# Kernel optimization log

Measured on AMD Instinct MI355X. Metric: run time of the kernel, lower is better.

Reference implementation:

```python
import jax, jax.numpy as jnp
import numpy as np

Q_LATTICE = 4      # nested lattice alphabet size
QMAX_ACT = 127.0   # 2**(8-1) - 1 for 8-bit LSQ


def _lattice_quantize(x_blocks, G, Ginv, q):
    # x_blocks: [N, 8] rows are block vectors. Lattice point = z @ G, z integer.
    z = jnp.round(x_blocks @ Ginv)
    half = q // 2
    z_mod = jnp.mod(z + half, q) - half  # nested (mod-q) lattice, centered
    return z_mod @ G


def setup_inputs() -> dict:
    key = jax.random.key(0)
    k1, k2 = jax.random.split(key)
    O, I, BS = 4096, 4096, 8
    rng = np.random.default_rng(0)
    G_np = np.eye(BS, dtype=np.float64) + 0.1 * rng.standard_normal((BS, BS))
    Ginv_np = np.linalg.inv(G_np)
    return {
        "x": jax.random.normal(k1, (256, I), dtype=jnp.float32),
        "weight": jax.random.normal(k2, (O, I), dtype=jnp.float32),
        "bias": jnp.zeros((O,), dtype=jnp.float32),
        "theta_beta": jnp.ones((O, 1), dtype=jnp.float32),
        "alpha": jnp.ones((1,), dtype=jnp.float32),
        "G": jnp.asarray(G_np, dtype=jnp.float32),
        "Ginv": jnp.asarray(Ginv_np, dtype=jnp.float32),
    }


def reference(x, weight, bias, theta_beta, alpha, G, Ginv):
    O, I = weight.shape
    bs = G.shape[0]
    nblk = I // bs
    sg = jax.lax.stop_gradient

    # --- hierarchical nested-lattice weight quantization (row tiling) ---
    W_blocks = weight.reshape(O, nblk, bs)
    # theta_beta [O, k] -> mean over k -> [O, 1, 1], broadcast to all blocks
    scale_w = jnp.mean(theta_beta, axis=-1, keepdims=True)[:, None, :]
    W_scaled = (W_blocks * scale_w).reshape(-1, bs)
    # straight-through lattice quantize
    W_q = W_scaled + sg(_lattice_quantize(W_scaled, G, Ginv, Q_LATTICE) - W_scaled)
    W_q = W_q.reshape(O, I)

    # --- linear ---
    y = x @ W_q.T + bias

    # --- LSQ activation quantization ---
    a = jax.nn.relu(alpha) + 1e-8          # [1]
    y_clipped = y + sg(jnp.clip(y, -a, a) - y)  # ste_clip (clamp detached)
    s = a / QMAX_ACT
    y_scaled = y_clipped / s
    y_round = y_scaled + sg(jnp.round(y_scaled) - y_scaled)  # ste_round
    return y_round * s
```

## Files before the change

kernel.cpp:

```cpp
#include <hip/hip_runtime.h>

typedef __attribute__((ext_vector_type(8))) __bf16 bf16x8;
typedef __attribute__((ext_vector_type(4))) float f32x4;

#define M_ 256
#define N_ 4096
#define K_ 4096
#define SPLITK 4
#define KC (K_ / SPLITK)
#define BM 128
#define BN 64
#define BK 32
#define KSTEPS (KC / BK)



__device__ __forceinline__ unsigned short f2bf(float f) {
  unsigned int u = __builtin_bit_cast(unsigned int, f);
  u += 0x7fffu + ((u >> 16) & 1u);
  return (unsigned short)(u >> 16);
}

__device__ __forceinline__ float lsq1(float y, float a, float s) {
  float yc = fminf(fmaxf(y, -a), a);
  return rintf(yc / s) * s;
}

__device__ __forceinline__ bf16x8 zdec_pk(unsigned int w) {
  unsigned int d0, d1, d2, d3;
#define ZP(P, D)                                                        \
  {                                                                     \
    const float f0 = (float)((w >> (4 * P)) & 3u) - 2.0f;               \
    const float f1 = (float)((w >> (4 * P + 2)) & 3u) - 2.0f;           \
    asm("v_cvt_pk_bf16_f32 %0, %1, %2" : "=v"(D) : "v"(f0), "v"(f1));   \
  }
  ZP(0, d0) ZP(1, d1) ZP(2, d2) ZP(3, d3)
#undef ZP
  const uint4 u = make_uint4(d0, d1, d2, d3);
  return __builtin_bit_cast(bf16x8, u);
}


#define NQB ((N_ * K_ / 8) / 256)
#define NXB ((M_ * K_ / 8) / 256)

__global__ __launch_bounds__(256) void k_prep(const float* __restrict__ W,
                                              const float* __restrict__ theta,
                                              const float* __restrict__ Ginv,
                                              const float* __restrict__ x,
                                              const float* __restrict__ G,
                                              unsigned short* __restrict__ z2,
                                              unsigned short* __restrict__ hi,
                                              unsigned short* __restrict__ lo,
                                              int kTheta) {
  __shared__ float Ms[64];
  const int tid = threadIdx.x;
  const bool isQ = blockIdx.x < NQB;
  if (tid < 64) Ms[tid] = isQ ? Ginv[tid] : G[tid];
  __syncthreads();

  if (isQ) {
#pragma clang fp contract(off)
    const int s = blockIdx.x * 256 + tid;
    const int lane6 = s & 63;
    const int tile = s >> 6;
    const int o  = ((tile >> 7) << 4) + (lane6 & 15);
    const int kb = ((tile & 127) << 2) + (lane6 >> 4);
    const float4* wp = (const float4*)(W + ((size_t)o << 12) + ((size_t)kb << 3));
    const float4 w0 = wp[0], w1 = wp[1];
    float sc = 0.f;
    for (int t = 0; t < kTheta; ++t) sc += theta[o * kTheta + t];
    sc /= (float)kTheta;
    const float wsv[8] = {w0.x * sc, w0.y * sc, w0.z * sc, w0.w * sc,
                          w1.x * sc, w1.y * sc, w1.z * sc, w1.w * sc};
    unsigned int word = 0u;
#pragma unroll
    for (int i = 0; i < 8; ++i) {
      float t = 0.f;
#pragma unroll
      for (int j = 0; j < 8; ++j)
        t = t + wsv[j] * Ms[j * 8 + i];
      const int zi = (int)rintf(t);
      word |= (unsigned int)((zi + 2) & 3) << (2 * i);
    }
    z2[s] = (unsigned short)word;
  } else {
    const int s = (blockIdx.x - NQB) * 256 + tid;
    const int lane6 = s & 63;
    const int tile = s >> 6;
    const int m  = ((tile >> 7) << 4) + (lane6 & 15);
    const int kb = ((tile & 127) << 2) + (lane6 >> 4);
    const float4* xp = (const float4*)(x + ((size_t)m << 12) + ((size_t)kb << 3));
    const float4 a0 = xp[0], a1 = xp[1];
    float xv[8] = {a0.x, a0.y, a0.z, a0.w, a1.x, a1.y, a1.z, a1.w};
    unsigned int ph[4] = {0u, 0u, 0u, 0u}, pl[4] = {0u, 0u, 0u, 0u};
#pragma unroll
    for (int i = 0; i < 8; ++i) {
      float t = 0.f;
#pragma unroll
      for (int j = 0; j < 8; ++j) t = fmaf(xv[j], Ms[i * 8 + j], t);
      const unsigned short hb = f2bf(t);
      const float hf = __builtin_bit_cast(float, (unsigned int)hb << 16);
      const unsigned short lb = f2bf(t - hf);
      ph[i >> 1] |= ((unsigned int)hb) << ((i & 1) * 16);
      pl[i >> 1] |= ((unsigned int)lb) << ((i & 1) * 16);
    }
    *(uint4*)(hi + ((size_t)s << 3)) = make_uint4(ph[0], ph[1], ph[2], ph[3]);
    *(uint4*)(lo + ((size_t)s << 3)) = make_uint4(pl[0], pl[1], pl[2], pl[3]);
  }
}


__global__ __launch_bounds__(512, 2) void k_gemm(const unsigned short* __restrict__ xgh,
                                                 const unsigned short* __restrict__ xgl,
                                                 const unsigned short* __restrict__ z2,
                                                 float* __restrict__ part) {
  const int tid = threadIdx.x;
  const int lane = tid & 63, wave = tid >> 6;
  const int wr = wave >> 1, wc = wave & 1;
  const int b = blockIdx.x;
  const int mt = b & 1;
  const int sk = (b >> 1) & 3;
  const int nt = b >> 3;
  const int k0t = sk * (KC / 32);
  const int lrow = lane & 15, lkg = lane >> 4;

  const unsigned short* ab[2];
  const unsigned short* lb2[2];
#pragma unroll
  for (int mf = 0; mf < 2; ++mf) {
    const size_t t = (size_t)((mt * 8 + wr * 2 + mf) * 128 + k0t);
    ab[mf]  = xgh + (t << 9) + lane * 8;
    lb2[mf] = xgl + (t << 9) + lane * 8;
  }
  const unsigned short* zb[2];
#pragma unroll
  for (int nf = 0; nf < 2; ++nf)
    zb[nf] = z2 + (((size_t)((nt * 4 + wc * 2 + nf) * 128 + k0t)) << 6) + lane;

  f32x4 acc[2][2] = {};

  bf16x8 cah[2], cal[2];
  unsigned int czw[2];
#pragma unroll
  for (int mf = 0; mf < 2; ++mf) {
    cah[mf] = *(const bf16x8*)(ab[mf]);
    cal[mf] = *(const bf16x8*)(lb2[mf]);
  }
#pragma unroll
  for (int nf = 0; nf < 2; ++nf) czw[nf] = zb[nf][0];

  for (int ks = 0; ks < KSTEPS; ++ks) {
    bf16x8 nah[2], nal[2];
    unsigned int nzw[2];
    if (ks + 1 < KSTEPS) {
#pragma unroll
      for (int mf = 0; mf < 2; ++mf) {
        nah[mf] = *(const bf16x8*)(ab[mf] + (size_t)(ks + 1) * 512);
        nal[mf] = *(const bf16x8*)(lb2[mf] + (size_t)(ks + 1) * 512);
      }
#pragma unroll
      for (int nf = 0; nf < 2; ++nf) nzw[nf] = zb[nf][(size_t)(ks + 1) * 64];
    } else {
#pragma unroll
      for (int mf = 0; mf < 2; ++mf) { nah[mf] = cah[mf]; nal[mf] = cal[mf]; }
#pragma unroll
      for (int nf = 0; nf < 2; ++nf) nzw[nf] = czw[nf];
    }

    bf16x8 bfr[2];
#pragma unroll
    for (int nf = 0; nf < 2; ++nf) bfr[nf] = zdec_pk(czw[nf]);

#pragma unroll
    for (int mf = 0; mf < 2; ++mf)
#pragma unroll
      for (int nf = 0; nf < 2; ++nf) {
        acc[mf][nf] = __builtin_amdgcn_mfma_f32_16x16x32_bf16(cah[mf], bfr[nf], acc[mf][nf], 0, 0, 0);
        acc[mf][nf] = __builtin_amdgcn_mfma_f32_16x16x32_bf16(cal[mf], bfr[nf], acc[mf][nf], 0, 0, 0);
      }

#pragma unroll
    for (int mf = 0; mf < 2; ++mf) { cah[mf] = nah[mf]; cal[mf] = nal[mf]; }
#pragma unroll
    for (int nf = 0; nf < 2; ++nf) czw[nf] = nzw[nf];
  }

  float* pb = part + (size_t)sk * (M_ * N_);
#pragma unroll
  for (int mf = 0; mf < 2; ++mf)
#pragma unroll
    for (int nf = 0; nf < 2; ++nf)
#pragma unroll
      for (int r = 0; r < 4; ++r) {
        const int m = mt * BM + wr * 32 + mf * 16 + lkg * 4 + r;
        const int n = nt * BN + wc * 32 + nf * 16 + lrow;
        pb[(size_t)m * N_ + n] = acc[mf][nf][r];
      }
}


__global__ __launch_bounds__(256) void k_epi(const float* __restrict__ part,
                                             const float* __restrict__ bias,
                                             const float* __restrict__ alpha,
                                             float* __restrict__ out) {
  const int i4 = blockIdx.x * 256 + threadIdx.x;
  const size_t off = (size_t)i4 * 4;
  const float4 p0 = *(const float4*)(part + off);
  const float4 p1 = *(const float4*)(part + (size_t)1 * M_ * N_ + off);
  const float4 p2 = *(const float4*)(part + (size_t)2 * M_ * N_ + off);
  const float4 p3 = *(const float4*)(part + (size_t)3 * M_ * N_ + off);
  const int n = (int)(off & (N_ - 1));
  const float4 bv = *(const float4*)(bias + n);
  const float a = fmaxf(alpha[0], 0.f) + 1e-8f;
  const float s = a / 127.0f;
  float4 o;
  o.x = lsq1(((p0.x + p1.x) + p2.x) + p3.x + bv.x, a, s);
  o.y = lsq1(((p0.y + p1.y) + p2.y) + p3.y + bv.y, a, s);
  o.z = lsq1(((p0.z + p1.z) + p2.z) + p3.z + bv.z, a, s);
  o.w = lsq1(((p0.w + p1.w) + p2.w) + p3.w + bv.w, a, s);
  *(float4*)(out + off) = o;
}


extern "C" void kernel_launch(void* const* d_in, const int* in_sizes, int n_in,
                              void* d_out, int out_size, void* d_ws, size_t ws_size,
                              hipStream_t stream) {
  const float* x     = (const float*)d_in[0];
  const float* W     = (const float*)d_in[1];
  const float* bias  = (const float*)d_in[2];
  const float* theta = (const float*)d_in[3];
  const float* alpha = (const float*)d_in[4];
  const float* G     = (const float*)d_in[5];
  const float* Ginv  = (const float*)d_in[6];
  float* out = (float*)d_out;

  const int O = in_sizes[2];
  const int kTheta = in_sizes[3] / O;

  char* ws = (char*)d_ws;
  unsigned short* xgh = (unsigned short*)ws;
  unsigned short* xgl = (unsigned short*)(ws + 2097152);
  unsigned short* z2  = (unsigned short*)(ws + 4194304);
  float* part = (float*)(ws + 8388608);
  if (ws_size < 25165824) return;

  k_prep<<<NQB + NXB, 256, 0, stream>>>(W, theta, Ginv, x, G, z2, xgh, xgl, kTheta);
  k_gemm<<<2 * SPLITK * 64, 512, 0, stream>>>(xgh, xgl, z2, part);
  k_epi<<<(M_ * N_ / 4) / 256, 256, 0, stream>>>(part, bias, alpha, out);
}
```

Baseline: 51.24 us.

## Drop split-K and fuse bias/LSQ epilogue into GEMM kernel

```diff
diff --git a/kernel.cpp b/kernel.cpp
--- a/kernel.cpp
+++ b/kernel.cpp
@@ -6,12 +6,10 @@
 #define M_ 256
 #define N_ 4096
 #define K_ 4096
-#define SPLITK 4
-#define KC (K_ / SPLITK)
-#define BM 128
+#define BM 64
 #define BN 64
-#define BK 32
-#define KSTEPS (KC / BK)
+#define NSTEP 128
+#define QSTEP 32
 
 
 
@@ -114,112 +112,73 @@
 __global__ __launch_bounds__(512, 2) void k_gemm(const unsigned short* __restrict__ xgh,
                                                  const unsigned short* __restrict__ xgl,
                                                  const unsigned short* __restrict__ z2,
-                                                 float* __restrict__ part) {
+                                                 const float* __restrict__ bias,
+                                                 const float* __restrict__ alpha,
+                                                 float* __restrict__ out) {
   const int tid = threadIdx.x;
   const int lane = tid & 63, wave = tid >> 6;
   const int wr = wave >> 1, wc = wave & 1;
   const int b = blockIdx.x;
-  const int mt = b & 1;
-  const int sk = (b >> 1) & 3;
-  const int nt = b >> 3;
-  const int k0t = sk * (KC / 32);
+  const int mt = b & 3;
+  const int nt = b >> 2;
   const int lrow = lane & 15, lkg = lane >> 4;
 
-  const unsigned short* ab[2];
-  const unsigned short* lb2[2];
-#pragma unroll
-  for (int mf = 0; mf < 2; ++mf) {
-    const size_t t = (size_t)((mt * 8 + wr * 2 + mf) * 128 + k0t);
-    ab[mf]  = xgh + (t << 9) + lane * 8;
-    lb2[mf] = xgl + (t << 9) + lane * 8;
-  }
+  const size_t ta = (size_t)((mt * 4 + wr) * 128) << 9;
+  const unsigned short* ah_p = xgh + ta + lane * 8;
+  const unsigned short* al_p = xgl + ta + lane * 8;
   const unsigned short* zb[2];
 #pragma unroll
   for (int nf = 0; nf < 2; ++nf)
-    zb[nf] = z2 + (((size_t)((nt * 4 + wc * 2 + nf) * 128 + k0t)) << 6) + lane;
-
-  f32x4 acc[2][2] = {};
-
-  bf16x8 cah[2], cal[2];
-  unsigned int czw[2];
-#pragma unroll
-  for (int mf = 0; mf < 2; ++mf) {
-    cah[mf] = *(const bf16x8*)(ab[mf]);
-    cal[mf] = *(const bf16x8*)(lb2[mf]);
-  }
-#pragma unroll
-  for (int nf = 0; nf < 2; ++nf) czw[nf] = zb[nf][0];
-
-  for (int ks = 0; ks < KSTEPS; ++ks) {
-    bf16x8 nah[2], nal[2];
-    unsigned int nzw[2];
-    if (ks + 1 < KSTEPS) {
-#pragma unroll
-      for (int mf = 0; mf < 2; ++mf) {
-        nah[mf] = *(const bf16x8*)(ab[mf] + (size_t)(ks + 1) * 512);
-        nal[mf] = *(const bf16x8*)(lb2[mf] + (size_t)(ks + 1) * 512);
+    zb[nf] = z2 + (((size_t)((nt * 4 + wc * 2 + nf) * 128)) << 6) + lane;
+
+  f32x4 acc[4][2] = {};
+
+  bf16x8 cah = *(const bf16x8*)(ah_p);
+  bf16x8 cal = *(const bf16x8*)(al_p);
+  unsigned int czw[2] = {zb[0][0], zb[1][0]};
+
+#pragma unroll
+  for (int q = 0; q < 4; ++q) {
+    for (int t = 0; t < QSTEP; ++t) {
+      const int ks = q * QSTEP + t;
+      bf16x8 nah, nal;
+      unsigned int nzw[2];
+      if (ks + 1 < NSTEP) {
+        nah = *(const bf16x8*)(ah_p + (size_t)(ks + 1) * 512);
+        nal = *(const bf16x8*)(al_p + (size_t)(ks + 1) * 512);
+        nzw[0] = zb[0][(size_t)(ks + 1) * 64];
+        nzw[1] = zb[1][(size_t)(ks + 1) * 64];
+      } else {
+        nah = cah; nal = cal; nzw[0] = czw[0]; nzw[1] = czw[1];
       }
-#pragma unroll
-      for (int nf = 0; nf < 2; ++nf) nzw[nf] = zb[nf][(size_t)(ks + 1) * 64];
-    } else {
-#pragma unroll
-      for (int mf = 0; mf < 2; ++mf) { nah[mf] = cah[mf]; nal[mf] = cal[mf]; }
-#pragma unroll
-      for (int nf = 0; nf < 2; ++nf) nzw[nf] = czw[nf];
-    }
-
-    bf16x8 bfr[2];
-#pragma unroll
-    for (int nf = 0; nf < 2; ++nf) bfr[nf] = zdec_pk(czw[nf]);
-
-#pragma unroll
-    for (int mf = 0; mf < 2; ++mf)
+
+      bf16x8 bfr[2];
+#pragma unroll
+      for (int nf = 0; nf < 2; ++nf) bfr[nf] = zdec_pk(czw[nf]);
+
 #pragma unroll
       for (int nf = 0; nf < 2; ++nf) {
-        acc[mf][nf] = __builtin_amdgcn_mfma_f32_16x16x32_bf16(cah[mf], bfr[nf], acc[mf][nf], 0, 0, 0);
-        acc[mf][nf] = __builtin_amdgcn_mfma_f32_16x16x32_bf16(cal[mf], bfr[nf], acc[mf][nf], 0, 0, 0);
+        acc[q][nf] = __builtin_amdgcn_mfma_f32_16x16x32_bf16(cah, bfr[nf], acc[q][nf], 0, 0, 0);
+        acc[q][nf] = __builtin_amdgcn_mfma_f32_16x16x32_bf16(cal, bfr[nf], acc[q][nf], 0, 0, 0);
       }
 
-#pragma unroll
-    for (int mf = 0; mf < 2; ++mf) { cah[mf] = nah[mf]; cal[mf] = nal[mf]; }
-#pragma unroll
-    for (int nf = 0; nf < 2; ++nf) czw[nf] = nzw[nf];
-  }
-
-  float* pb = part + (size_t)sk * (M_ * N_);
-#pragma unroll
-  for (int mf = 0; mf < 2; ++mf)
-#pragma unroll
-    for (int nf = 0; nf < 2; ++nf)
-#pragma unroll
-      for (int r = 0; r < 4; ++r) {
-        const int m = mt * BM + wr * 32 + mf * 16 + lkg * 4 + r;
-        const int n = nt * BN + wc * 32 + nf * 16 + lrow;
-        pb[(size_t)m * N_ + n] = acc[mf][nf][r];
-      }
-}
-
-
-__global__ __launch_bounds__(256) void k_epi(const float* __restrict__ part,
-                                             const float* __restrict__ bias,
-                                             const float* __restrict__ alpha,
-                                             float* __restrict__ out) {
-  const int i4 = blockIdx.x * 256 + threadIdx.x;
-  const size_t off = (size_t)i4 * 4;
-  const float4 p0 = *(const float4*)(part + off);
-  const float4 p1 = *(const float4*)(part + (size_t)1 * M_ * N_ + off);
-  const float4 p2 = *(const float4*)(part + (size_t)2 * M_ * N_ + off);
-  const float4 p3 = *(const float4*)(part + (size_t)3 * M_ * N_ + off);
-  const int n = (int)(off & (N_ - 1));
-  const float4 bv = *(const float4*)(bias + n);
+      cah = nah; cal = nal; czw[0] = nzw[0]; czw[1] = nzw[1];
+    }
+  }
+
   const float a = fmaxf(alpha[0], 0.f) + 1e-8f;
   const float s = a / 127.0f;
-  float4 o;
-  o.x = lsq1(((p0.x + p1.x) + p2.x) + p3.x + bv.x, a, s);
-  o.y = lsq1(((p0.y + p1.y) + p2.y) + p3.y + bv.y, a, s);
-  o.z = lsq1(((p0.z + p1.z) + p2.z) + p3.z + bv.z, a, s);
-  o.w = lsq1(((p0.w + p1.w) + p2.w) + p3.w + bv.w, a, s);
-  *(float4*)(out + off) = o;
+#pragma unroll
+  for (int nf = 0; nf < 2; ++nf) {
+    const int n = nt * BN + wc * 32 + nf * 16 + lrow;
+    const float bv = bias[n];
+#pragma unroll
+    for (int r = 0; r < 4; ++r) {
+      const int m = mt * BM + wr * 16 + lkg * 4 + r;
+      const float y = ((acc[0][nf][r] + acc[1][nf][r]) + acc[2][nf][r]) + acc[3][nf][r] + bv;
+      out[(size_t)m * N_ + n] = lsq1(y, a, s);
+    }
+  }
 }
 
 
@@ -242,10 +201,8 @@
   unsigned short* xgh = (unsigned short*)ws;
   unsigned short* xgl = (unsigned short*)(ws + 2097152);
   unsigned short* z2  = (unsigned short*)(ws + 4194304);
-  float* part = (float*)(ws + 8388608);
-  if (ws_size < 25165824) return;
+  if (ws_size < 8388608) return;
 
   k_prep<<<NQB + NXB, 256, 0, stream>>>(W, theta, Ginv, x, G, z2, xgh, xgl, kTheta);
-  k_gemm<<<2 * SPLITK * 64, 512, 0, stream>>>(xgh, xgl, z2, part);
-  k_epi<<<(M_ * N_ / 4) / 256, 256, 0, stream>>>(part, bias, alpha, out);
-}
+  k_gemm<<<4 * (N_ / BN), 512, 0, stream>>>(xgh, xgl, z2, bias, alpha, out);
+}
```

Result: slower. 71.84 us (+40.2%).
